# Kernel tuning notes

Hardware: AMD Instinct MI355X
Metric: run time of the kernel (lower is better)

The kernel has to match this reference:

```python
import jax, jax.numpy as jnp
import numpy as np

RADIUS = 0.1
K = 32  # num_neighbors


def _ball_query(points, centers, radius, k):
    # points: [B,3,N], centers: [B,3,M] -> indices [B,M,K] (int32)
    # PVCNN semantics: first k point indices within radius of each center,
    # unfilled slots padded with the first in-ball index (0 if none in ball).
    N = points.shape[-1]
    p2 = jnp.sum(points * points, axis=1)            # [B,N]
    c2 = jnp.sum(centers * centers, axis=1)          # [B,M]
    cp = jnp.einsum('bdm,bdn->bmn', centers, points)  # [B,M,N]
    dist2 = c2[:, :, None] + p2[:, None, :] - 2.0 * cp
    valid = dist2 < radius * radius                  # [B,M,N]
    # score = point index if in ball else sentinel N; sorting ascending puts
    # the first k in-ball indices (in original point order) up front.
    scores = jnp.where(valid, jnp.arange(N, dtype=jnp.int32), jnp.int32(N))
    idx = jnp.sort(scores, axis=-1)[..., :k]         # [B,M,K]
    first = idx[..., :1]
    first = jnp.where(first == N, 0, first)          # no neighbor -> index 0
    return jnp.where(idx == N, first, idx)


def _group(feat, idx):
    # feat: [B,C,N], idx: [B,M,K] -> [B,C,M,K]
    return jnp.take_along_axis(feat[:, :, None, :], idx[:, None, :, :], axis=3)


def setup_inputs() -> dict:
    key = jax.random.key(0)
    k1, k2, k3 = jax.random.split(key, 3)
    B, N, M, C = 2, 16384, 4096, 32
    points_coords = jax.random.uniform(k1, (B, 3, N), dtype=jnp.float32)
    centers_coords = jax.random.uniform(k2, (B, 3, M), dtype=jnp.float32)
    points_features = jax.random.normal(k3, (B, C, N), dtype=jnp.float32)
    return {
        'points_coords': points_coords,
        'centers_coords': centers_coords,
        'points_features': points_features,
    }


def reference(points_coords, centers_coords, points_features):
    idx = _ball_query(points_coords, centers_coords, RADIUS, K)     # [B,M,K]
    nbr_coords = _group(points_coords, idx)                          # [B,3,M,K]
    nbr_coords = nbr_coords - centers_coords[:, :, :, None]         # relative
    nbr_feats = _group(points_features, idx)                         # [B,C,M,K]
    out = jnp.concatenate([nbr_coords, nbr_feats], axis=1)          # [B,3+C,M,K]
    return jnp.transpose(out, (0, 1, 3, 2))                          # [B,3+C,K,M]
```

## Files before the change

kernel.cpp:

```cpp
#include <hip/hip_runtime.h>

#define B_SZ  2
#define N_PTS 16384
#define M_CTR 4096
#define C_FT  32
#define K_NB  32
#define NCH   35
#define CH_STRIDE (K_NB * M_CTR)
#define CELLS 10
#define NCELL (CELLS * CELLS * CELLS)

typedef float vfloat2 __attribute__((ext_vector_type(2)));

__device__ __forceinline__ float fmul(float a, float b) {
    float r; asm("v_mul_f32 %0, %1, %2" : "=v"(r) : "v"(a), "v"(b)); return r;
}
__device__ __forceinline__ float fadd(float a, float b) {
    float r; asm("v_add_f32 %0, %1, %2" : "=v"(r) : "v"(a), "v"(b)); return r;
}
__device__ __forceinline__ float fsub(float a, float b) {
    float r; asm("v_sub_f32 %0, %1, %2" : "=v"(r) : "v"(a), "v"(b)); return r;
}
__device__ __forceinline__ float ffma(float a, float b, float c) {
    float r; asm("v_fma_f32 %0, %1, %2, %3" : "=v"(r) : "v"(a), "v"(b), "v"(c));
    return r;
}

__device__ __forceinline__ bool bq_valid(float x, float y, float z,
                                         float cx, float cy, float cz,
                                         float c2, float r2) {
    const float p2 = fadd(fadd(fmul(x, x), fmul(y, y)), fmul(z, z));
    const float cp = ffma(cz, z, ffma(cy, y, fmul(cx, x)));
    return fsub(fadd(c2, p2), fmul(2.0f, cp)) < r2;
}

__device__ __forceinline__ int cell_of(float x, float y, float z) {
    int ci = (int)(x * 10.0f); ci = ci < 0 ? 0 : (ci > 9 ? 9 : ci);
    int cj = (int)(y * 10.0f); cj = cj < 0 ? 0 : (cj > 9 ? 9 : cj);
    int ck = (int)(z * 10.0f); ck = ck < 0 ? 0 : (ck > 9 ? 9 : ck);
    return (ck * CELLS + cj) * CELLS + ci;
}

__global__ __launch_bounds__(1024) void prep_kernel(
    const float* __restrict__ points,
    const float* __restrict__ feats,
    int* __restrict__ starts,
    int* __restrict__ cursor,
    float* __restrict__ pf)
{
    if (blockIdx.x < B_SZ) {
        const int b = blockIdx.x;
        const int t = threadIdx.x;
        const int lane = t & 63, wid = t >> 6;
        __shared__ int h[NCELL];
        __shared__ int wsum[16];
        for (int c = t; c < NCELL; c += 1024) h[c] = 0;
        __syncthreads();

        const float* __restrict__ px = points + (b * 3 + 0) * N_PTS;
        const float* __restrict__ py = points + (b * 3 + 1) * N_PTS;
        const float* __restrict__ pz = points + (b * 3 + 2) * N_PTS;
#pragma unroll
        for (int i = 0; i < 16; ++i) {
            const int n = t + i * 1024;
            atomicAdd(&h[cell_of(px[n], py[n], pz[n])], 1);
        }
        __syncthreads();

        const int v = (t < NCELL) ? h[t] : 0;
        int incl = v;
        for (int off = 1; off < 64; off <<= 1) {
            const int u = __shfl_up(incl, off);
            if (lane >= off) incl += u;
        }
        if (lane == 63) wsum[wid] = incl;
        __syncthreads();
        if (wid == 0 && lane < 16) {
            const int s = wsum[lane];
            int in2 = s;
            for (int off = 1; off < 16; off <<= 1) {
                const int u = __shfl_up(in2, off);
                if (lane >= off) in2 += u;
            }
            wsum[lane] = in2 - s;
        }
        __syncthreads();
        if (t < NCELL) {
            const int excl = incl - v + wsum[wid];
            starts[b * (NCELL + 1) + t] = excl;
            cursor[b * NCELL + t] = excl;
            if (t == NCELL - 1) starts[b * (NCELL + 1) + NCELL] = excl + v;
        }
    } else {
        __shared__ float tile[64][37];
        const int bid = blockIdx.x - B_SZ;
        const int t  = threadIdx.x;
        const int b  = bid >> 8;
        const int n0 = (bid & 255) * 64;
        for (int i = t; i < NCH * 64; i += 1024) {
            const int r = i >> 6;
            const int c = i & 63;
            float v;
            if (r < 3) v = points[(b * 3 + r) * N_PTS + n0 + c];
            else       v = feats[(b * C_FT + (r - 3)) * N_PTS + n0 + c];
            tile[c][r] = v;
        }
        if (t < 64) tile[t][35] = 0.0f;
        __syncthreads();
        float* __restrict__ dst = pf + ((size_t)b * N_PTS + n0) * 36;
        for (int o = t; o < 64 * 36; o += 1024) {
            const int c = o / 36;
            const int r = o - c * 36;
            dst[o] = tile[c][r];
        }
    }
}

__global__ __launch_bounds__(256) void scatter_kernel(
    const float* __restrict__ points, int* __restrict__ cursor,
    float4* __restrict__ binned) {
    const int t = blockIdx.x * 256 + threadIdx.x;
    const int b = t >> 14, n = t & (N_PTS - 1);
    const float x = points[(b * 3 + 0) * N_PTS + n];
    const float y = points[(b * 3 + 1) * N_PTS + n];
    const float z = points[(b * 3 + 2) * N_PTS + n];
    const int pos = atomicAdd(&cursor[b * NCELL + cell_of(x, y, z)], 1);
    binned[b * N_PTS + pos] = make_float4(x, y, z, __int_as_float(n));
}

__global__ __launch_bounds__(256) void ball_query_kernel(
    const float4* __restrict__ binned,
    const float* __restrict__ centers,
    const int* __restrict__ starts,
    int* __restrict__ idx_out)
{
    const int lane = threadIdx.x & 63;
    const int wid  = threadIdx.x >> 6;
    const int cid  = blockIdx.x * 4 + wid;
    const int b = cid >> 12;
    const int m = cid & (M_CTR - 1);

    const float r2 = (float)(0.1 * 0.1);

    const float cx = centers[(b * 3 + 0) * M_CTR + m];
    const float cy = centers[(b * 3 + 1) * M_CTR + m];
    const float cz = centers[(b * 3 + 2) * M_CTR + m];
    const float c2 = fadd(fadd(fmul(cx, cx), fmul(cy, cy)), fmul(cz, cz));

    __shared__ unsigned bitmap[4][N_PTS / 32];
    unsigned* bm = bitmap[wid];
#pragma unroll
    for (int j = 0; j < 8; ++j) bm[j * 64 + lane] = 0u;

    int ci = (int)(cx * 10.0f); ci = ci < 0 ? 0 : (ci > 9 ? 9 : ci);
    int cj = (int)(cy * 10.0f); cj = cj < 0 ? 0 : (cj > 9 ? 9 : cj);
    int ck = (int)(cz * 10.0f); ck = ck < 0 ? 0 : (ck > 9 ? 9 : ck);
    ci = __builtin_amdgcn_readfirstlane(ci);
    cj = __builtin_amdgcn_readfirstlane(cj);
    ck = __builtin_amdgcn_readfirstlane(ck);
    const int i0 = ci > 0 ? ci - 1 : 0;
    const int i1 = ci < 9 ? ci + 1 : 9;
    const int* st = starts + b * (NCELL + 1);
    const float4* __restrict__ bp = binned + b * N_PTS;

    int lo_d[9], hi_d[9];
#pragma unroll
    for (int d = 0; d < 9; ++d) {
        const int jj = cj + (d % 3) - 1;
        const int kk = ck + (d / 3) - 1;
        const bool ok = (jj >= 0) & (jj <= 9) & (kk >= 0) & (kk <= 9);
        const int base = ok ? (kk * CELLS + jj) * CELLS : 0;
        const int lo = st[base + i0];
        const int hi = st[base + i1 + 1];
        lo_d[d] = ok ? lo : 0;
        hi_d[d] = ok ? hi : 0;
    }

#pragma unroll
    for (int d = 0; d < 9; ++d) {
        const int lo = lo_d[d];
        const int hi = hi_d[d];
        for (int s0 = lo; s0 < hi; s0 += 64) {
            const int t = s0 + lane;
            if (t < hi) {
                const float4 p = bp[t];
                if (bq_valid(p.x, p.y, p.z, cx, cy, cz, c2, r2)) {
                    const int n = __float_as_int(p.w);
                    atomicOr((int*)&bm[(((n >> 5) & 7) << 6) + (n >> 8)],
                             1 << (n & 31));
                }
            }
        }
    }

    unsigned w[8];
    int cnt = 0;
#pragma unroll
    for (int j = 0; j < 8; ++j) {
        w[j] = bm[j * 64 + lane];
        cnt += __popc(w[j]);
    }

    int incl = cnt;
    for (int off = 1; off < 64; off <<= 1) {
        const int v = __shfl_up(incl, off);
        if (lane >= off) incl += v;
    }
    const int total = __shfl(incl, 63);
    int slot = incl - cnt;

    int firstbit = 0x7fffffff;
#pragma unroll
    for (int j = 0; j < 8; ++j) {
        if (w[j] && firstbit == 0x7fffffff)
            firstbit = lane * 256 + j * 32 + (__ffs(w[j]) - 1);
    }
    for (int off = 32; off > 0; off >>= 1)
        firstbit = min(firstbit, __shfl_xor(firstbit, off));
    const int first_idx = (total == 0) ? 0 : firstbit;

    int* __restrict__ dst = idx_out + (b * K_NB) * M_CTR + m;
#pragma unroll
    for (int j = 0; j < 8; ++j) {
        unsigned x = w[j];
        while (x && slot < K_NB) {
            const int bit = __ffs(x) - 1;
            dst[slot * M_CTR] = lane * 256 + j * 32 + bit;
            x &= x - 1;
            ++slot;
        }
    }
    if (lane >= total && lane < K_NB) dst[lane * M_CTR] = first_idx;
}

__global__ __launch_bounds__(256) void gather_kernel(
    const float* __restrict__ pf,
    const float* __restrict__ centers,
    const int* __restrict__ idx,
    float* __restrict__ out)
{
    const int t = blockIdx.x * 256 + threadIdx.x;
    const int m = (t & (M_CTR / 2 - 1)) * 2;
    const int k = (t >> 11) & (K_NB - 1);
    const int b = t >> 16;

    const int2 nn = *(const int2*)&idx[(b * K_NB + k) * M_CTR + m];
    const float4* __restrict__ s0 =
        (const float4*)(pf + ((size_t)b * N_PTS + nn.x) * 36);
    const float4* __restrict__ s1 =
        (const float4*)(pf + ((size_t)b * N_PTS + nn.y) * 36);

    float4 f0[9], f1[9];
#pragma unroll
    for (int i = 0; i < 9; ++i) { f0[i] = s0[i]; f1[i] = s1[i]; }

    const float2 cx = *(const float2*)&centers[(b * 3 + 0) * M_CTR + m];
    const float2 cy = *(const float2*)&centers[(b * 3 + 1) * M_CTR + m];
    const float2 cz = *(const float2*)&centers[(b * 3 + 2) * M_CTR + m];

    float v0[36], v1[36];
#pragma unroll
    for (int i = 0; i < 9; ++i) {
        v0[4 * i + 0] = f0[i].x; v0[4 * i + 1] = f0[i].y;
        v0[4 * i + 2] = f0[i].z; v0[4 * i + 3] = f0[i].w;
        v1[4 * i + 0] = f1[i].x; v1[4 * i + 1] = f1[i].y;
        v1[4 * i + 2] = f1[i].z; v1[4 * i + 3] = f1[i].w;
    }
    v0[0] -= cx.x; v0[1] -= cy.x; v0[2] -= cz.x;
    v1[0] -= cx.y; v1[1] -= cy.y; v1[2] -= cz.y;

    float* __restrict__ o = out + ((size_t)b * NCH * K_NB + k) * M_CTR + m;
#pragma unroll
    for (int ch = 0; ch < NCH; ++ch) {
        vfloat2 pv; pv.x = v0[ch]; pv.y = v1[ch];
        __builtin_nontemporal_store(pv, (vfloat2*)&o[(size_t)ch * CH_STRIDE]);
    }
}

extern "C" void kernel_launch(void* const* d_in, const int* in_sizes, int n_in,
                              void* d_out, int out_size, void* d_ws, size_t ws_size,
                              hipStream_t stream) {
    const float* points  = (const float*)d_in[0];
    const float* centers = (const float*)d_in[1];
    const float* feats   = (const float*)d_in[2];
    float* out = (float*)d_out;

    char* ws = (char*)d_ws;
    int*    idx    = (int*)ws;
    float*  pf     = (float*)(ws + (1u << 20));
    int*    cursor = (int*)(ws + 5716 * 1024);
    int*    starts = (int*)(ws + 5732 * 1024);
    float4* binned = (float4*)(ws + 5764 * 1024);

    prep_kernel<<<B_SZ + B_SZ * (N_PTS / 64), 1024, 0, stream>>>(
        points, feats, starts, cursor, pf);
    scatter_kernel<<<(B_SZ * N_PTS) / 256, 256, 0, stream>>>(
        points, cursor, binned);
    ball_query_kernel<<<(B_SZ * M_CTR) / 4, 256, 0, stream>>>(
        binned, centers, starts, idx);
    gather_kernel<<<(B_SZ * K_NB * M_CTR / 2) / 256, 256, 0, stream>>>(
        pf, centers, idx, out);
}
```

Measured before the change: 104.3 us.

## Fuse scatter into prep kernel and remap blocks to XCDs by batch

Drops the separate scatter kernel. The histogram blocks in prep_kernel now keep the cell ids in registers, turn the shared histogram into cursors after the scan, and scatter points into the binned array using shared-memory atomics instead of global ones. This saves one kernel launch and the global cursor traffic. Separately, ball_query and gather remap block indices so that blocks on the same XCD (blockIdx mod 8) work on one batch, which aims for better L2 locality. The trade-off is that the two batch blocks now do the whole scatter serially, 16K points each, on only two CUs.

After: 114.3 us. +9.6%, slower.

```diff
diff --git a/kernel.cpp b/kernel.cpp
--- a/kernel.cpp
+++ b/kernel.cpp
@@ -45,7 +45,7 @@
     const float* __restrict__ points,
     const float* __restrict__ feats,
     int* __restrict__ starts,
-    int* __restrict__ cursor,
+    float4* __restrict__ binned,
     float* __restrict__ pf)
 {
     if (blockIdx.x < B_SZ) {
@@ -60,10 +60,12 @@
         const float* __restrict__ px = points + (b * 3 + 0) * N_PTS;
         const float* __restrict__ py = points + (b * 3 + 1) * N_PTS;
         const float* __restrict__ pz = points + (b * 3 + 2) * N_PTS;
+        int cells[16];
 #pragma unroll
         for (int i = 0; i < 16; ++i) {
             const int n = t + i * 1024;
-            atomicAdd(&h[cell_of(px[n], py[n], pz[n])], 1);
+            cells[i] = cell_of(px[n], py[n], pz[n]);
+            atomicAdd(&h[cells[i]], 1);
         }
         __syncthreads();
 
@@ -88,8 +90,18 @@
         if (t < NCELL) {
             const int excl = incl - v + wsum[wid];
             starts[b * (NCELL + 1) + t] = excl;
-            cursor[b * NCELL + t] = excl;
+            h[t] = excl;
             if (t == NCELL - 1) starts[b * (NCELL + 1) + NCELL] = excl + v;
+        }
+        __syncthreads();
+
+        float4* __restrict__ bb = binned + b * N_PTS;
+#pragma unroll
+        for (int i = 0; i < 16; ++i) {
+            const int n = t + i * 1024;
+            const float x = px[n], y = py[n], z = pz[n];
+            const int pos = atomicAdd(&h[cells[i]], 1);
+            bb[pos] = make_float4(x, y, z, __int_as_float(n));
         }
     } else {
         __shared__ float tile[64][37];
@@ -116,18 +128,6 @@
     }
 }
 
-__global__ __launch_bounds__(256) void scatter_kernel(
-    const float* __restrict__ points, int* __restrict__ cursor,
-    float4* __restrict__ binned) {
-    const int t = blockIdx.x * 256 + threadIdx.x;
-    const int b = t >> 14, n = t & (N_PTS - 1);
-    const float x = points[(b * 3 + 0) * N_PTS + n];
-    const float y = points[(b * 3 + 1) * N_PTS + n];
-    const float z = points[(b * 3 + 2) * N_PTS + n];
-    const int pos = atomicAdd(&cursor[b * NCELL + cell_of(x, y, z)], 1);
-    binned[b * N_PTS + pos] = make_float4(x, y, z, __int_as_float(n));
-}
-
 __global__ __launch_bounds__(256) void ball_query_kernel(
     const float4* __restrict__ binned,
     const float* __restrict__ centers,
@@ -136,9 +136,10 @@
 {
     const int lane = threadIdx.x & 63;
     const int wid  = threadIdx.x >> 6;
-    const int cid  = blockIdx.x * 4 + wid;
-    const int b = cid >> 12;
-    const int m = cid & (M_CTR - 1);
+    const int xcd  = blockIdx.x & 7;
+    const int b    = xcd >> 2;
+    const int u    = (blockIdx.x >> 3) * 4 + (xcd & 3);
+    const int m    = u * 4 + wid;
 
     const float r2 = (float)(0.1 * 0.1);
 
@@ -239,10 +240,12 @@
     const int* __restrict__ idx,
     float* __restrict__ out)
 {
-    const int t = blockIdx.x * 256 + threadIdx.x;
-    const int m = (t & (M_CTR / 2 - 1)) * 2;
-    const int k = (t >> 11) & (K_NB - 1);
-    const int b = t >> 16;
+    const int xcd = blockIdx.x & 7;
+    const int b   = xcd >> 2;
+    const int u   = (blockIdx.x >> 3) * 4 + (xcd & 3);
+    const int g   = u * 256 + threadIdx.x;
+    const int m = (g & (M_CTR / 2 - 1)) * 2;
+    const int k = g >> 11;
 
     const int2 nn = *(const int2*)&idx[(b * K_NB + k) * M_CTR + m];
     const float4* __restrict__ s0 =
@@ -288,14 +291,11 @@
     char* ws = (char*)d_ws;
     int*    idx    = (int*)ws;
     float*  pf     = (float*)(ws + (1u << 20));
-    int*    cursor = (int*)(ws + 5716 * 1024);
     int*    starts = (int*)(ws + 5732 * 1024);
     float4* binned = (float4*)(ws + 5764 * 1024);
 
     prep_kernel<<<B_SZ + B_SZ * (N_PTS / 64), 1024, 0, stream>>>(
-        points, feats, starts, cursor, pf);
-    scatter_kernel<<<(B_SZ * N_PTS) / 256, 256, 0, stream>>>(
-        points, cursor, binned);
+        points, feats, starts, binned, pf);
     ball_query_kernel<<<(B_SZ * M_CTR) / 4, 256, 0, stream>>>(
         binned, centers, starts, idx);
     gather_kernel<<<(B_SZ * K_NB * M_CTR / 2) / 256, 256, 0, stream>>>(
```
